# Kernel optimization log

Hardware: AMD Instinct MI355X
Metric: run time of the kernel (lower is better)

## Reference

```python
import jax, jax.numpy as jnp
from jax import lax
import numpy as np

D_MODEL = 256; D_INNER = 512; D_STATE = 16; D_CONV = 4; DT_RANK = 16
B = 2; T = 4096


def _mamba(x, W_in, conv_w, conv_b, W_x, W_dt, b_dt, A_log, D, W_out):
    # Standard mamba_ssm Mamba block (d_state=16, d_conv=4, expand=2).
    b, t, _ = x.shape
    xz = x @ W_in                                   # (B,T,2*d_inner)
    xi, z = jnp.split(xz, 2, axis=-1)
    # causal depthwise conv1d along T
    xc = lax.conv_general_dilated(
        xi.transpose(0, 2, 1), conv_w[:, None, :], (1,),
        [(D_CONV - 1, 0)], dimension_numbers=('NCH', 'OIH', 'NCH'),
        feature_group_count=D_INNER)
    xi = jax.nn.silu(xc.transpose(0, 2, 1) + conv_b)  # (B,T,d_inner)
    xdbl = xi @ W_x                                  # (B,T,dt_rank+2*d_state)
    dt, Bm, Cm = jnp.split(xdbl, [DT_RANK, DT_RANK + D_STATE], axis=-1)
    dt = jax.nn.softplus(dt @ W_dt + b_dt)           # (B,T,d_inner)
    A = -jnp.exp(A_log)                              # (d_inner,d_state)
    dA = jnp.exp(dt[..., None] * A)                  # (B,T,d_inner,d_state)
    dBx = dt[..., None] * Bm[:, :, None, :] * xi[..., None]

    def step(h, ins):
        dA_t, dBx_t, C_t = ins
        h = dA_t * h + dBx_t                         # (B,d_inner,d_state)
        y = jnp.einsum('bdn,bn->bd', h, C_t)
        return h, y

    h0 = jnp.zeros((b, D_INNER, D_STATE), x.dtype)
    _, ys = lax.scan(step, h0,
                     (dA.transpose(1, 0, 2, 3), dBx.transpose(1, 0, 2, 3),
                      Cm.transpose(1, 0, 2)))
    y = ys.transpose(1, 0, 2) + xi * D               # skip connection D*x
    y = y * jax.nn.silu(z)                           # gate
    return y @ W_out                                 # (B,T,d_model)


def _mamba_params(key, prefix):
    ks = jax.random.split(key, 6)
    s = 0.02
    return {
        prefix + "_W_in": jax.random.normal(ks[0], (D_MODEL, 2 * D_INNER)) * s,
        prefix + "_conv_w": jax.random.normal(ks[1], (D_INNER, D_CONV)) * s,
        prefix + "_conv_b": jnp.zeros((D_INNER,), jnp.float32),
        prefix + "_W_x": jax.random.normal(ks[2], (D_INNER, DT_RANK + 2 * D_STATE)) * s,
        prefix + "_W_dt": jax.random.normal(ks[3], (DT_RANK, D_INNER)) * s,
        prefix + "_b_dt": jax.random.normal(ks[4], (D_INNER,)) * s,
        prefix + "_A_log": jnp.log(jnp.tile(jnp.arange(1, D_STATE + 1, dtype=jnp.float32), (D_INNER, 1))),
        prefix + "_D": jnp.ones((D_INNER,), jnp.float32),
        prefix + "_W_out": jax.random.normal(ks[5], (D_INNER, D_MODEL)) * s,
    }


def setup_inputs():
    key = jax.random.key(0)
    kx, kf, kb, km = jax.random.split(key, 4)
    inp = {"x": jax.random.normal(kx, (B, T, D_MODEL), jnp.float32)}
    inp.update(_mamba_params(kf, "fw"))
    inp.update(_mamba_params(kb, "bw"))
    inp["merge_W"] = jax.random.normal(km, (2 * D_MODEL, D_MODEL)) * 0.02
    return inp


def reference(x, fw_W_in, fw_conv_w, fw_conv_b, fw_W_x, fw_W_dt, fw_b_dt, fw_A_log, fw_D, fw_W_out,
              bw_W_in, bw_conv_w, bw_conv_b, bw_W_x, bw_W_dt, bw_b_dt, bw_A_log, bw_D, bw_W_out,
              merge_W):
    out_f = _mamba(x, fw_W_in, fw_conv_w, fw_conv_b, fw_W_x, fw_W_dt, fw_b_dt, fw_A_log, fw_D, fw_W_out)
    out_b = jnp.flip(
        _mamba(jnp.flip(x, 1), bw_W_in, bw_conv_w, bw_conv_b, bw_W_x, bw_W_dt, bw_b_dt, bw_A_log, bw_D, bw_W_out),
        1)
    # dropout is identity in eval mode
    return jnp.concatenate([out_f, out_b], axis=-1) @ merge_W
```

## Files before the change

kernel.cpp:

```cpp
#include <hip/hip_runtime.h>
#include <math.h>

#define T_SEQ 4096
#define ROWS 8192
#define NCHUNK 128
#define CLEN 32

typedef __attribute__((ext_vector_type(4))) float f32x4;
typedef __attribute__((ext_vector_type(2))) float f32x2;
typedef __attribute__((ext_vector_type(8))) short s16x8;

#if __has_builtin(__builtin_elementwise_fma)
#define PKFMA(a, b, c) __builtin_elementwise_fma((a), (b), (c))
#else
#define PKFMA(a, b, c) ((a) * (b) + (c))
#endif

__device__ __forceinline__ float siluf(float x) { return x / (1.f + __expf(-x)); }
__device__ __forceinline__ float softplusf(float x) {
    return fmaxf(x, 0.f) + __logf(1.f + __expf(-fabsf(x)));
}
__device__ __forceinline__ ushort f2b(float f) {
    uint u = __float_as_uint(f);
    u += 0x7fffu + ((u >> 16) & 1u);
    return (ushort)(u >> 16);
}
__device__ __forceinline__ float b2f(ushort h) { return __uint_as_float(((uint)h) << 16); }

__device__ __forceinline__ void gl16(const ushort* g, const char* l)
{
    __builtin_amdgcn_global_load_lds(
        (const __attribute__((address_space(1))) void*)g,
        (__attribute__((address_space(3))) void*)l,
        16, 0, 0);
}

__device__ __forceinline__ void cvt_body(const float* in, ushort* out, int bid, int tid)
{
    int i = bid * 256 + tid;
    const float4* p = reinterpret_cast<const float4*>(in) + (size_t)i * 2;
    float4 a = p[0], b = p[1];
    s16x8 v;
    v[0] = (short)f2b(a.x); v[1] = (short)f2b(a.y); v[2] = (short)f2b(a.z); v[3] = (short)f2b(a.w);
    v[4] = (short)f2b(b.x); v[5] = (short)f2b(b.y); v[6] = (short)f2b(b.z); v[7] = (short)f2b(b.w);
    *reinterpret_cast<s16x8*>(out + (size_t)i * 8) = v;
}

__device__ __forceinline__ void transpose_body(const float* W, ushort* WT,
                                               int Kdim, int Ndim, int bid, int tid)
{
    int idx = bid * 256 + tid;
    int kg8 = Kdim >> 3;
    if (idx >= Ndim * kg8) return;
    int n = idx / kg8, kg = idx - n * kg8;
    s16x8 v;
    #pragma unroll
    for (int i = 0; i < 8; ++i)
        v[i] = (short)f2b(W[(size_t)(kg * 8 + i) * Ndim + n]);
    *reinterpret_cast<s16x8*>(WT + (size_t)n * Kdim + kg * 8) = v;
}

__device__ __forceinline__ void fusew_body(const float* W_out, const float* merge,
                                           ushort* WT, int mrow0, int koff, int bid, int tid)
{
    int idx = bid * 256 + tid;
    int dd = idx >> 8, j = idx & 255;
    float acc = 0.f;
    const float* wr = W_out + dd * 256;
    const float* mc = merge + (size_t)mrow0 * 256 + j;
    #pragma unroll 4
    for (int m = 0; m < 256; ++m)
        acc = fmaf(wr[m], mc[(size_t)m * 256], acc);
    WT[(size_t)j * 1024 + koff + dd] = f2b(acc);
}

__device__ __forceinline__ void wall_body(const float* Wx, const float* Wdt,
                                          ushort* WT, int bid, int tid)
{
    int idx = bid * 256 + tid;
    int n = idx >> 6, kg = idx & 63;
    s16x8 v;
    #pragma unroll
    for (int i = 0; i < 8; ++i) {
        int k = kg * 8 + i;
        float acc = 0.f;
        if (n < 512) {
            #pragma unroll
            for (int j = 0; j < 16; ++j)
                acc = fmaf(Wx[k * 48 + j], Wdt[j * 512 + n], acc);
        } else if (n < 544) {
            acc = Wx[k * 48 + 16 + (n - 512)];
        }
        v[i] = (short)f2b(acc);
    }
    *reinterpret_cast<s16x8*>(WT + (size_t)n * 512 + kg * 8) = v;
}

__global__ __launch_bounds__(256)
void prep_kernel(const float* __restrict__ x,
                 const float* __restrict__ fW_in, const float* __restrict__ bW_in,
                 const float* __restrict__ fW_out, const float* __restrict__ bW_out,
                 const float* __restrict__ merge,
                 const float* __restrict__ fW_x, const float* __restrict__ fW_dt,
                 const float* __restrict__ bW_x, const float* __restrict__ bW_dt,
                 ushort* __restrict__ xbh,
                 ushort* __restrict__ WinT_f, ushort* __restrict__ WinT_b,
                 ushort* __restrict__ WallOut,
                 ushort* __restrict__ Wall_f, ushort* __restrict__ Wall_b)
{
    int bid = blockIdx.x, tid = threadIdx.x;
    if (bid < 1024)        cvt_body(x, xbh, bid, tid);
    else if (bid < 1152)   transpose_body(fW_in, WinT_f, 256, 1024, bid - 1024, tid);
    else if (bid < 1280)   transpose_body(bW_in, WinT_b, 256, 1024, bid - 1152, tid);
    else if (bid < 1792)   fusew_body(fW_out, merge, WallOut, 0, 0, bid - 1280, tid);
    else if (bid < 2304)   fusew_body(bW_out, merge, WallOut, 256, 512, bid - 1792, tid);
    else if (bid < 2464)   wall_body(fW_x, fW_dt, Wall_f, bid - 2304, tid);
    else                   wall_body(bW_x, bW_dt, Wall_b, bid - 2464, tid);
}

template<int BM, int BN, int EPI>
__global__ __launch_bounds__(256)
void mgemm(const ushort* __restrict__ A0, const ushort* __restrict__ A1,
           const ushort* __restrict__ B0, const ushort* __restrict__ B1,
           void* __restrict__ C0, void* __restrict__ C1,
           const float* __restrict__ bias0, const float* __restrict__ bias1,
           float* __restrict__ X0, float* __restrict__ X1,
           int K, int ldc, int flip0, int flip1, int zmode, int nseg)
{
    constexpr int MF = BM / 32, NF = BN / 32;
    constexpr int ASTR = BM / 32, BSTR = BN / 32;
    constexpr int ABYTES = BM * 128;
    __shared__ char lds[BM * 128 + BN * 128];

    const int tid = threadIdx.x;
    const int L = tid & 63, w = tid >> 6;
    const int wm = w >> 1, wn = w & 1;
    const int m0 = blockIdx.y * BM, n0 = blockIdx.x * BN;

    f32x4 acc[MF][NF];
    #pragma unroll
    for (int i = 0; i < MF; ++i)
        #pragma unroll
        for (int j = 0; j < NF; ++j)
            acc[i][j] = (f32x4){0.f, 0.f, 0.f, 0.f};

    const int rsub = L >> 3;
    const int q = (L & 7) ^ rsub;
    const int sb = zmode ? blockIdx.z : 0;
    const int se = zmode ? sb + 1 : nseg;

    for (int s = sb; s < se; ++s) {
        const ushort* Ap = s ? A1 : A0;
        const ushort* Bp = s ? B1 : B0;
        const int flip = s ? flip1 : flip0;

        const ushort* ap[ASTR];
        const ushort* bp[BSTR];
        #pragma unroll
        for (int c = 0; c < ASTR; ++c) {
            int rg = m0 + (w * ASTR + c) * 8 + rsub;
            if (flip) rg ^= (T_SEQ - 1);
            ap[c] = Ap + (size_t)rg * K + q * 8;
        }
        #pragma unroll
        for (int c = 0; c < BSTR; ++c) {
            int ng = n0 + (w * BSTR + c) * 8 + rsub;
            bp[c] = Bp + (size_t)ng * K + q * 8;
        }

        for (int k0 = 0; k0 < K; k0 += 64) {
            #pragma unroll
            for (int c = 0; c < ASTR; ++c) {
                gl16(ap[c], lds + (w * ASTR + c) * 1024);
                ap[c] += 64;
            }
            #pragma unroll
            for (int c = 0; c < BSTR; ++c) {
                gl16(bp[c], lds + ABYTES + (w * BSTR + c) * 1024);
                bp[c] += 64;
            }
            __syncthreads();
            #pragma unroll
            for (int kk = 0; kk < 2; ++kk) {
                const int sw = (((kk * 4 + (L >> 4)) ^ (L & 7)) << 4);
                s16x8 af[MF], bf[NF];
                #pragma unroll
                for (int i = 0; i < MF; ++i) {
                    int R = wm * (BM / 2) + i * 16 + (L & 15);
                    af[i] = *reinterpret_cast<const s16x8*>(lds + R * 128 + sw);
                }
                #pragma unroll
                for (int j = 0; j < NF; ++j) {
                    int R = wn * (BN / 2) + j * 16 + (L & 15);
                    bf[j] = *reinterpret_cast<const s16x8*>(lds + ABYTES + R * 128 + sw);
                }
                #pragma unroll
                for (int i = 0; i < MF; ++i)
                    #pragma unroll
                    for (int j = 0; j < NF; ++j)
                        acc[i][j] = __builtin_amdgcn_mfma_f32_16x16x32_bf16(
                            af[i], bf[j], acc[i][j], 0, 0, 0);
            }
            __syncthreads();
        }
    }

    void* Cv = (zmode && blockIdx.z) ? C1 : C0;
    const float* bias = (zmode && blockIdx.z) ? bias1 : bias0;
    float* Xv = (zmode && blockIdx.z) ? X1 : X0;
    #pragma unroll
    for (int i = 0; i < MF; ++i) {
        #pragma unroll
        for (int j = 0; j < NF; ++j) {
            int r0 = m0 + wm * (BM / 2) + i * 16 + ((L >> 4) << 2);
            int c  = n0 + wn * (BN / 2) + j * 16 + (L & 15);
            if (EPI == 2) {
                if (c < 512) {
                    float bv = bias[c];
                    #pragma unroll
                    for (int r = 0; r < 4; ++r)
                        ((float*)Cv)[(size_t)(r0 + r) * 512 + c] =
                            softplusf(acc[i][j][r] + bv);
                } else if (c < 544) {
                    #pragma unroll
                    for (int r = 0; r < 4; ++r)
                        Xv[(size_t)(r0 + r) * 32 + (c - 512)] = acc[i][j][r];
                }
            } else {
                #pragma unroll
                for (int r = 0; r < 4; ++r) {
                    size_t o = (size_t)(r0 + r) * ldc + c;
                    if (EPI == 1) ((ushort*)Cv)[o] = f2b(acc[i][j][r]);
                    else          ((float*)Cv)[o]  = acc[i][j][r];
                }
            }
        }
    }
}

__global__ __launch_bounds__(256)
void conv_kernel(const ushort* __restrict__ xz_f, const ushort* __restrict__ xz_b,
                 const float* __restrict__ w_f, const float* __restrict__ w_b,
                 const float* __restrict__ bias_f, const float* __restrict__ bias_b,
                 ushort* __restrict__ xi_f, ushort* __restrict__ xi_b)
{
    int g = blockIdx.x * 256 + threadIdx.x;
    int dir = g >> 17;
    int rem = g & 131071;
    int rb = rem >> 7;
    int cg = rem & 127;
    int r0 = rb * 8;
    int d0 = cg * 4;
    int t0 = r0 & (T_SEQ - 1);

    const ushort* xz  = dir ? xz_b : xz_f;
    const float*  w   = dir ? w_b : w_f;
    const float*  bia = dir ? bias_b : bias_f;
    ushort*       xi  = dir ? xi_b : xi_f;

    float wv[4][4], bs[4];
    #pragma unroll
    for (int j = 0; j < 4; ++j) {
        float4 wj = *reinterpret_cast<const float4*>(w + (d0 + j) * 4);
        wv[j][0] = wj.x; wv[j][1] = wj.y; wv[j][2] = wj.z; wv[j][3] = wj.w;
        bs[j] = bia[d0 + j];
    }

    float xv[11][4];
    #pragma unroll
    for (int k = 0; k < 11; ++k) {
        int tt = t0 - 3 + k;
        if (tt >= 0) {
            ushort4 v = *reinterpret_cast<const ushort4*>(
                xz + (size_t)(r0 - 3 + k) * 1024 + d0);
            xv[k][0] = b2f(v.x); xv[k][1] = b2f(v.y);
            xv[k][2] = b2f(v.z); xv[k][3] = b2f(v.w);
        } else {
            xv[k][0] = xv[k][1] = xv[k][2] = xv[k][3] = 0.f;
        }
    }

    #pragma unroll
    for (int t = 0; t < 8; ++t) {
        ushort4 o;
        ushort* op = reinterpret_cast<ushort*>(&o);
        #pragma unroll
        for (int j = 0; j < 4; ++j) {
            float acc = bs[j];
            acc = fmaf(wv[j][0], xv[t + 0][j], acc);
            acc = fmaf(wv[j][1], xv[t + 1][j], acc);
            acc = fmaf(wv[j][2], xv[t + 2][j], acc);
            acc = fmaf(wv[j][3], xv[t + 3][j], acc);
            op[j] = f2b(siluf(acc));
        }
        *reinterpret_cast<ushort4*>(xi + (size_t)(r0 + t) * 512 + d0) = o;
    }
}

__device__ __forceinline__ void scan_head(int bid, int tid,
    int& db, int& b, int& dir, int& chunk, int& d, size_t& row0)
{
    int half = bid & 1;
    int tmp = bid >> 1;
    chunk = tmp & (NCHUNK - 1);
    db = tmp >> 7;
    b = db & 1; dir = db >> 1;
    d = half * 256 + tid;
    row0 = (size_t)b * T_SEQ + (size_t)chunk * CLEN;
}

__device__ __forceinline__ void load_a16(const float* __restrict__ Al, int d,
                                         float* a, bool& fast)
{
    const float4* ap = reinterpret_cast<const float4*>(Al + (size_t)d * 16);
    #pragma unroll
    for (int i = 0; i < 4; ++i) {
        float4 v = ap[i];
        a[4*i+0] = -expf(v.x); a[4*i+1] = -expf(v.y);
        a[4*i+2] = -expf(v.z); a[4*i+3] = -expf(v.w);
    }
    fast = true;
    #pragma unroll
    for (int n = 1; n < 16; ++n)
        fast = fast && (fabsf(a[n] - (float)(n + 1) * a[0]) <= 1e-4f * (float)(n + 1));
}

#define LD16(dst, src_t)                                              \
    {                                                                 \
        const float4* q_ = reinterpret_cast<const float4*>(src_t);    \
        float4 q0 = q_[0], q1 = q_[1], q2 = q_[2], q3 = q_[3];        \
        dst[0]=q0.x; dst[1]=q0.y; dst[2]=q0.z; dst[3]=q0.w;           \
        dst[4]=q1.x; dst[5]=q1.y; dst[6]=q1.z; dst[7]=q1.w;           \
        dst[8]=q2.x; dst[9]=q2.y; dst[10]=q2.z; dst[11]=q2.w;         \
        dst[12]=q3.x; dst[13]=q3.y; dst[14]=q3.z; dst[15]=q3.w;       \
    }

__global__ __launch_bounds__(256)
void scan_pass1(const ushort* __restrict__ xi_f, const ushort* __restrict__ xi_b,
                const float* __restrict__ dt_f, const float* __restrict__ dt_b,
                const float* __restrict__ xd_f, const float* __restrict__ xd_b,
                const float* __restrict__ Al_f, const float* __restrict__ Al_b,
                float* __restrict__ Sdt, float* __restrict__ Hloc)
{
    __shared__ float Bsh[CLEN][16];
    int db, b, dir, chunk, d; size_t row0;
    scan_head(blockIdx.x, threadIdx.x, db, b, dir, chunk, d, row0);

    const ushort* xi = dir ? xi_b : xi_f;
    const float* dt  = dir ? dt_b : dt_f;
    const float* xd  = dir ? xd_b : xd_f;
    const float* Al  = dir ? Al_b : Al_f;

    float a[16]; bool fast;
    load_a16(Al, d, a, fast);

    for (int i = threadIdx.x; i < CLEN * 16; i += 256) {
        int r = i >> 4, n = i & 15;
        Bsh[r][n] = xd[(row0 + r) * 32 + n];
    }
    __syncthreads();

    const ushort* xip = xi + row0 * 512 + d;
    const float*  dtp = dt + row0 * 512 + d;
    float h[16];
    float sumdt = 0.f;

    if (fast) {
        f32x2 h2[8];
        #pragma unroll
        for (int j = 0; j < 8; ++j) h2[j] = (f32x2){0.f, 0.f};
        for (int t = 0; t < CLEN; ++t) {
            float dtv = dtp[(size_t)t * 512];
            float xiv = b2f(xip[(size_t)t * 512]);
            float dbx = dtv * xiv;
            sumdt += dtv;
            float qv = __expf(dtv * a[0]);
            float q2 = qv * qv;
            f32x2 Q2 = (f32x2){q2, q2};
            f32x2 p  = (f32x2){qv, q2};
            f32x2 dbx2 = (f32x2){dbx, dbx};
            const f32x2* bq = reinterpret_cast<const f32x2*>(Bsh[t]);
            #pragma unroll
            for (int j = 0; j < 8; ++j) {
                f32x2 r = bq[j] * dbx2;
                h2[j] = PKFMA(p, h2[j], r);
                if (j < 7) p = p * Q2;
            }
        }
        #pragma unroll
        for (int j = 0; j < 8; ++j) { h[2*j] = h2[j][0]; h[2*j+1] = h2[j][1]; }
    } else {
        #pragma unroll
        for (int n = 0; n < 16; ++n) h[n] = 0.f;
        for (int t = 0; t < CLEN; ++t) {
            float bn[16]; LD16(bn, Bsh[t]);
            float dtv = dtp[(size_t)t * 512];
            float xiv = b2f(xip[(size_t)t * 512]);
            float dbx = dtv * xiv;
            sumdt += dtv;
            #pragma unroll
            for (int n = 0; n < 16; ++n) {
                float dA = __expf(dtv * a[n]);
                h[n] = fmaf(dA, h[n], dbx * bn[n]);
            }
        }
    }

    Sdt[((size_t)db * NCHUNK + chunk) * 512 + d] = sumdt;
    size_t si = ((size_t)((db * NCHUNK + chunk) * 512 + d)) * 16;
    float4* Ho = reinterpret_cast<float4*>(Hloc + si);
    #pragma unroll
    for (int i = 0; i < 4; ++i)
        Ho[i] = make_float4(h[4*i+0], h[4*i+1], h[4*i+2], h[4*i+3]);
}

__global__ __launch_bounds__(256)
void scan_pass2(const float* __restrict__ Sdt, const float* __restrict__ Hloc,
                const float* __restrict__ Al_f, const float* __restrict__ Al_b,
                float* __restrict__ Hin)
{
    int tid = blockIdx.x * 256 + threadIdx.x;
    int db = tid >> 13;
    int dn = tid & 8191;
    int d = dn >> 4;
    const float* Al = (db >> 1) ? Al_b : Al_f;
    float a = -expf(Al[dn]);

    size_t hbase = (size_t)db * NCHUNK * 8192 + dn;
    size_t sbase = (size_t)db * NCHUNK * 512 + d;
    float h = 0.f;
    #pragma unroll 4
    for (int c = 0; c < NCHUNK; ++c) {
        Hin[hbase + (size_t)c * 8192] = h;
        float dA = __expf(a * Sdt[sbase + (size_t)c * 512]);
        h = fmaf(dA, h, Hloc[hbase + (size_t)c * 8192]);
    }
}

__global__ __launch_bounds__(256)
void scan_pass3(const ushort* __restrict__ xi_f, const ushort* __restrict__ xi_b,
                const float* __restrict__ dt_f, const float* __restrict__ dt_b,
                const float* __restrict__ xd_f, const float* __restrict__ xd_b,
                const float* __restrict__ Al_f, const float* __restrict__ Al_b,
                const ushort* __restrict__ xz_f, const ushort* __restrict__ xz_b,
                const float* __restrict__ D_f, const float* __restrict__ D_b,
                const float* __restrict__ Hin,
                ushort* __restrict__ y_all)
{
    __shared__ float Bsh[CLEN][16];
    __shared__ float Csh[CLEN][16];
    int db, b, dir, chunk, d; size_t row0;
    scan_head(blockIdx.x, threadIdx.x, db, b, dir, chunk, d, row0);

    const ushort* xi = dir ? xi_b : xi_f;
    const float* dt  = dir ? dt_b : dt_f;
    const float* xd  = dir ? xd_b : xd_f;
    const float* Al  = dir ? Al_b : Al_f;
    const ushort* xz = dir ? xz_b : xz_f;
    const float* Dv  = dir ? D_b  : D_f;

    float a[16]; bool fast;
    load_a16(Al, d, a, fast);
    float Dd = Dv[d];

    for (int i = threadIdx.x; i < CLEN * 32; i += 256) {
        int r = i >> 5, c = i & 31;
        float v = xd[(row0 + r) * 32 + c];
        if (c < 16) Bsh[r][c] = v; else Csh[r][c - 16] = v;
    }
    __syncthreads();

    const ushort* xip = xi + row0 * 512 + d;
    const float*  dtp = dt + row0 * 512 + d;
    const ushort* zp  = xz + row0 * 1024 + 512 + d;

    ushort* yp;
    long ystep;
    if (dir == 0) {
        yp = y_all + row0 * 1024 + d;
        ystep = 1024;
    } else {
        size_t rowu = (size_t)b * T_SEQ + (T_SEQ - 1) - (size_t)chunk * CLEN;
        yp = y_all + rowu * 1024 + 512 + d;
        ystep = -1024;
    }

    size_t si = ((size_t)((db * NCHUNK + chunk) * 512 + d)) * 16;

    if (fast) {
        f32x2 h2[8];
        {
            const f32x2* hp = reinterpret_cast<const f32x2*>(Hin + si);
            #pragma unroll
            for (int j = 0; j < 8; ++j) h2[j] = hp[j];
        }
        for (int t = 0; t < CLEN; ++t) {
            float dtv = dtp[(size_t)t * 512];
            float xiv = b2f(xip[(size_t)t * 512]);
            float zv  = b2f(zp[(size_t)t * 1024]);
            float dbx = dtv * xiv;
            float qv = __expf(dtv * a[0]);
            float q2 = qv * qv;
            f32x2 Q2 = (f32x2){q2, q2};
            f32x2 p  = (f32x2){qv, q2};
            f32x2 dbx2 = (f32x2){dbx, dbx};
            f32x2 yac = (f32x2){0.f, 0.f};
            const f32x2* bq = reinterpret_cast<const f32x2*>(Bsh[t]);
            const f32x2* cq = reinterpret_cast<const f32x2*>(Csh[t]);
            #pragma unroll
            for (int j = 0; j < 8; ++j) {
                f32x2 r = bq[j] * dbx2;
                h2[j] = PKFMA(p, h2[j], r);
                yac = PKFMA(h2[j], cq[j], yac);
                if (j < 7) p = p * Q2;
            }
            float yacc = yac[0] + yac[1];
            yp[(long)t * ystep] = f2b(fmaf(xiv, Dd, yacc) * siluf(zv));
        }
    } else {
        float h[16];
        {
            const float4* hp = reinterpret_cast<const float4*>(Hin + si);
            #pragma unroll
            for (int i = 0; i < 4; ++i) {
                float4 v = hp[i];
                h[4*i+0] = v.x; h[4*i+1] = v.y; h[4*i+2] = v.z; h[4*i+3] = v.w;
            }
        }
        for (int t = 0; t < CLEN; ++t) {
            float bn[16]; LD16(bn, Bsh[t]);
            float cn[16]; LD16(cn, Csh[t]);
            float dtv = dtp[(size_t)t * 512];
            float xiv = b2f(xip[(size_t)t * 512]);
            float zv  = b2f(zp[(size_t)t * 1024]);
            float dbx = dtv * xiv;
            float yacc = 0.f;
            #pragma unroll
            for (int n = 0; n < 16; ++n) {
                float dA = __expf(dtv * a[n]);
                h[n] = fmaf(dA, h[n], dbx * bn[n]);
                yacc = fmaf(h[n], cn[n], yacc);
            }
            yp[(long)t * ystep] = f2b(fmaf(xiv, Dd, yacc) * siluf(zv));
        }
    }
}

extern "C" void kernel_launch(void* const* d_in, const int* in_sizes, int n_in,
                              void* d_out, int out_size, void* d_ws, size_t ws_size,
                              hipStream_t stream)
{
    const float* x       = (const float*)d_in[0];
    const float* fW_in   = (const float*)d_in[1];
    const float* fconv_w = (const float*)d_in[2];
    const float* fconv_b = (const float*)d_in[3];
    const float* fW_x    = (const float*)d_in[4];
    const float* fW_dt   = (const float*)d_in[5];
    const float* fb_dt   = (const float*)d_in[6];
    const float* fA_log  = (const float*)d_in[7];
    const float* fD      = (const float*)d_in[8];
    const float* fW_out  = (const float*)d_in[9];
    const float* bW_in   = (const float*)d_in[10];
    const float* bconv_w = (const float*)d_in[11];
    const float* bconv_b = (const float*)d_in[12];
    const float* bW_x    = (const float*)d_in[13];
    const float* bW_dt   = (const float*)d_in[14];
    const float* bb_dt   = (const float*)d_in[15];
    const float* bA_log  = (const float*)d_in[16];
    const float* bD      = (const float*)d_in[17];
    const float* bW_out  = (const float*)d_in[18];
    const float* merge   = (const float*)d_in[19];
    float* out = (float*)d_out;

    char* ws = (char*)d_ws;
    ushort* xbh     = (ushort*)ws; ws += (size_t)ROWS * 256 * 2;
    ushort* WinT_f  = (ushort*)ws; ws += (size_t)1024 * 256 * 2;
    ushort* WinT_b  = (ushort*)ws; ws += (size_t)1024 * 256 * 2;
    ushort* WallOut = (ushort*)ws; ws += (size_t)256 * 1024 * 2;
    ushort* Wall_f  = (ushort*)ws; ws += (size_t)640 * 512 * 2;
    ushort* Wall_b  = (ushort*)ws; ws += (size_t)640 * 512 * 2;
    ushort* xz_f    = (ushort*)ws; ws += (size_t)ROWS * 1024 * 2;
    ushort* xz_b    = (ushort*)ws; ws += (size_t)ROWS * 1024 * 2;
    ushort* xi_f    = (ushort*)ws; ws += (size_t)ROWS * 512 * 2;
    ushort* xi_b    = (ushort*)ws; ws += (size_t)ROWS * 512 * 2;
    ushort* y_all   = (ushort*)ws; ws += (size_t)ROWS * 1024 * 2;
    float*  dt_f    = (float*)ws;  ws += (size_t)ROWS * 512 * 4;
    float*  dt_b    = (float*)ws;  ws += (size_t)ROWS * 512 * 4;
    float*  xd_f    = (float*)ws;  ws += (size_t)ROWS * 32 * 4;
    float*  xd_b    = (float*)ws;  ws += (size_t)ROWS * 32 * 4;
    float*  Sdt     = (float*)ws;  ws += (size_t)4 * NCHUNK * 512 * 4;
    float*  Hloc    = (float*)ws;  ws += (size_t)4 * NCHUNK * 8192 * 4;
    float*  Hin     = (float*)ws;  ws += (size_t)4 * NCHUNK * 8192 * 4;

    dim3 blk(256);

    prep_kernel<<<2624, blk, 0, stream>>>(x, fW_in, bW_in, fW_out, bW_out, merge,
                                          fW_x, fW_dt, bW_x, bW_dt,
                                          xbh, WinT_f, WinT_b, WallOut, Wall_f, Wall_b);

    mgemm<64, 128, 1><<<dim3(8, 128, 2), blk, 0, stream>>>(
        xbh, xbh, WinT_f, WinT_b, xz_f, xz_b, nullptr, nullptr, nullptr, nullptr,
        256, 1024, 0, 1, 1, 1);

    conv_kernel<<<1024, blk, 0, stream>>>(xz_f, xz_b, fconv_w, bconv_w,
                                          fconv_b, bconv_b, xi_f, xi_b);

    mgemm<64, 128, 2><<<dim3(5, 128, 2), blk, 0, stream>>>(
        xi_f, xi_b, Wall_f, Wall_b, dt_f, dt_b, fb_dt, bb_dt, xd_f, xd_b,
        512, 512, 0, 0, 1, 1);

    scan_pass1<<<1024, blk, 0, stream>>>(xi_f, xi_b, dt_f, dt_b, xd_f, xd_b,
                                         fA_log, bA_log, Sdt, Hloc);
    scan_pass2<<<128, blk, 0, stream>>>(Sdt, Hloc, fA_log, bA_log, Hin);
    scan_pass3<<<1024, blk, 0, stream>>>(xi_f, xi_b, dt_f, dt_b, xd_f, xd_b,
                                         fA_log, bA_log, xz_f, xz_b, fD, bD,
                                         Hin, y_all);

    mgemm<64, 64, 0><<<dim3(4, 128, 1), blk, 0, stream>>>(
        y_all, nullptr, WallOut, nullptr, out, nullptr, nullptr, nullptr,
        nullptr, nullptr, 1024, 256, 0, 0, 0, 1);
}
```

Before: 176.1 us.

## Store dt in bf16, merge in-proj GEMMs, and swizzle GEMM block order

The dt activation buffer becomes bf16 instead of fp32. The dt_proj GEMM epilogue writes bf16, and both scan passes convert it back to float on load, which halves dt traffic in three kernels. The forward and backward in_proj GEMMs become one N=2048 GEMM over the unflipped input. It relies on WinT_f and WinT_b sitting next to each other in memory, and the backward half is written to time-flipped rows. A linear block-index swizzle in mgemm groups neighbouring tiles differently, likely to improve cache locality across chiplets. The cost is lower dt precision feeding the exponentials in the scan.

```diff
diff --git a/kernel.cpp b/kernel.cpp
--- a/kernel.cpp
+++ b/kernel.cpp
@@ -135,7 +135,17 @@
     const int tid = threadIdx.x;
     const int L = tid & 63, w = tid >> 6;
     const int wm = w >> 1, wn = w & 1;
-    const int m0 = blockIdx.y * BM, n0 = blockIdx.x * BN;
+
+    const int nbx = gridDim.x, nby = gridDim.y;
+    int lin = blockIdx.x + nbx * (blockIdx.y + nby * blockIdx.z);
+    int nwg = nbx * nby * gridDim.z;
+    int swz = (lin & 7) * (nwg >> 3) + (lin >> 3);
+    int bz = swz / (nbx * nby);
+    int r2 = swz - bz * nbx * nby;
+    int by = r2 / nbx;
+    int bx = r2 - by * nbx;
+
+    const int m0 = by * BM, n0 = bx * BN;
 
     f32x4 acc[MF][NF];
     #pragma unroll
@@ -146,7 +156,7 @@
 
     const int rsub = L >> 3;
     const int q = (L & 7) ^ rsub;
-    const int sb = zmode ? blockIdx.z : 0;
+    const int sb = zmode ? bz : 0;
     const int se = zmode ? sb + 1 : nseg;
 
     for (int s = sb; s < se; ++s) {
@@ -205,9 +215,9 @@
         }
     }
 
-    void* Cv = (zmode && blockIdx.z) ? C1 : C0;
-    const float* bias = (zmode && blockIdx.z) ? bias1 : bias0;
-    float* Xv = (zmode && blockIdx.z) ? X1 : X0;
+    void* Cv = (zmode && bz) ? C1 : C0;
+    const float* bias = (zmode && bz) ? bias1 : bias0;
+    float* Xv = (zmode && bz) ? X1 : X0;
     #pragma unroll
     for (int i = 0; i < MF; ++i) {
         #pragma unroll
@@ -219,20 +229,28 @@
                     float bv = bias[c];
                     #pragma unroll
                     for (int r = 0; r < 4; ++r)
-                        ((float*)Cv)[(size_t)(r0 + r) * 512 + c] =
-                            softplusf(acc[i][j][r] + bv);
+                        ((ushort*)Cv)[(size_t)(r0 + r) * 512 + c] =
+                            f2b(softplusf(acc[i][j][r] + bv));
                 } else if (c < 544) {
                     #pragma unroll
                     for (int r = 0; r < 4; ++r)
                         Xv[(size_t)(r0 + r) * 32 + (c - 512)] = acc[i][j][r];
                 }
+            } else if (EPI == 3) {
+                if (c < 1024) {
+                    #pragma unroll
+                    for (int r = 0; r < 4; ++r)
+                        ((ushort*)C0)[(size_t)(r0 + r) * 1024 + c] = f2b(acc[i][j][r]);
+                } else {
+                    #pragma unroll
+                    for (int r = 0; r < 4; ++r)
+                        ((ushort*)C1)[(size_t)((r0 + r) ^ (T_SEQ - 1)) * 1024 + (c - 1024)] =
+                            f2b(acc[i][j][r]);
+                }
             } else {
                 #pragma unroll
-                for (int r = 0; r < 4; ++r) {
-                    size_t o = (size_t)(r0 + r) * ldc + c;
-                    if (EPI == 1) ((ushort*)Cv)[o] = f2b(acc[i][j][r]);
-                    else          ((float*)Cv)[o]  = acc[i][j][r];
-                }
+                for (int r = 0; r < 4; ++r)
+                    ((float*)Cv)[(size_t)(r0 + r) * ldc + c] = acc[i][j][r];
             }
         }
     }
@@ -337,7 +355,7 @@
 
 __global__ __launch_bounds__(256)
 void scan_pass1(const ushort* __restrict__ xi_f, const ushort* __restrict__ xi_b,
-                const float* __restrict__ dt_f, const float* __restrict__ dt_b,
+                const ushort* __restrict__ dt_f, const ushort* __restrict__ dt_b,
                 const float* __restrict__ xd_f, const float* __restrict__ xd_b,
                 const float* __restrict__ Al_f, const float* __restrict__ Al_b,
                 float* __restrict__ Sdt, float* __restrict__ Hloc)
@@ -347,7 +365,7 @@
     scan_head(blockIdx.x, threadIdx.x, db, b, dir, chunk, d, row0);
 
     const ushort* xi = dir ? xi_b : xi_f;
-    const float* dt  = dir ? dt_b : dt_f;
+    const ushort* dt = dir ? dt_b : dt_f;
     const float* xd  = dir ? xd_b : xd_f;
     const float* Al  = dir ? Al_b : Al_f;
 
@@ -361,7 +379,7 @@
     __syncthreads();
 
     const ushort* xip = xi + row0 * 512 + d;
-    const float*  dtp = dt + row0 * 512 + d;
+    const ushort* dtp = dt + row0 * 512 + d;
     float h[16];
     float sumdt = 0.f;
 
@@ -370,7 +388,7 @@
         #pragma unroll
         for (int j = 0; j < 8; ++j) h2[j] = (f32x2){0.f, 0.f};
         for (int t = 0; t < CLEN; ++t) {
-            float dtv = dtp[(size_t)t * 512];
+            float dtv = b2f(dtp[(size_t)t * 512]);
             float xiv = b2f(xip[(size_t)t * 512]);
             float dbx = dtv * xiv;
             sumdt += dtv;
@@ -394,7 +412,7 @@
         for (int n = 0; n < 16; ++n) h[n] = 0.f;
         for (int t = 0; t < CLEN; ++t) {
             float bn[16]; LD16(bn, Bsh[t]);
-            float dtv = dtp[(size_t)t * 512];
+            float dtv = b2f(dtp[(size_t)t * 512]);
             float xiv = b2f(xip[(size_t)t * 512]);
             float dbx = dtv * xiv;
             sumdt += dtv;
@@ -439,7 +457,7 @@
 
 __global__ __launch_bounds__(256)
 void scan_pass3(const ushort* __restrict__ xi_f, const ushort* __restrict__ xi_b,
-                const float* __restrict__ dt_f, const float* __restrict__ dt_b,
+                const ushort* __restrict__ dt_f, const ushort* __restrict__ dt_b,
                 const float* __restrict__ xd_f, const float* __restrict__ xd_b,
                 const float* __restrict__ Al_f, const float* __restrict__ Al_b,
                 const ushort* __restrict__ xz_f, const ushort* __restrict__ xz_b,
@@ -453,7 +471,7 @@
     scan_head(blockIdx.x, threadIdx.x, db, b, dir, chunk, d, row0);
 
     const ushort* xi = dir ? xi_b : xi_f;
-    const float* dt  = dir ? dt_b : dt_f;
+    const ushort* dt = dir ? dt_b : dt_f;
     const float* xd  = dir ? xd_b : xd_f;
     const float* Al  = dir ? Al_b : Al_f;
     const ushort* xz = dir ? xz_b : xz_f;
@@ -471,7 +489,7 @@
     __syncthreads();
 
     const ushort* xip = xi + row0 * 512 + d;
-    const float*  dtp = dt + row0 * 512 + d;
+    const ushort* dtp = dt + row0 * 512 + d;
     const ushort* zp  = xz + row0 * 1024 + 512 + d;
 
     ushort* yp;
@@ -495,7 +513,7 @@
             for (int j = 0; j < 8; ++j) h2[j] = hp[j];
         }
         for (int t = 0; t < CLEN; ++t) {
-            float dtv = dtp[(size_t)t * 512];
+            float dtv = b2f(dtp[(size_t)t * 512]);
             float xiv = b2f(xip[(size_t)t * 512]);
             float zv  = b2f(zp[(size_t)t * 1024]);
             float dbx = dtv * xiv;
@@ -530,7 +548,7 @@
         for (int t = 0; t < CLEN; ++t) {
             float bn[16]; LD16(bn, Bsh[t]);
             float cn[16]; LD16(cn, Csh[t]);
-            float dtv = dtp[(size_t)t * 512];
+            float dtv = b2f(dtp[(size_t)t * 512]);
             float xiv = b2f(xip[(size_t)t * 512]);
             float zv  = b2f(zp[(size_t)t * 1024]);
             float dbx = dtv * xiv;
@@ -584,8 +602,8 @@
     ushort* xi_f    = (ushort*)ws; ws += (size_t)ROWS * 512 * 2;
     ushort* xi_b    = (ushort*)ws; ws += (size_t)ROWS * 512 * 2;
     ushort* y_all   = (ushort*)ws; ws += (size_t)ROWS * 1024 * 2;
-    float*  dt_f    = (float*)ws;  ws += (size_t)ROWS * 512 * 4;
-    float*  dt_b    = (float*)ws;  ws += (size_t)ROWS * 512 * 4;
+    ushort* dt_f    = (ushort*)ws; ws += (size_t)ROWS * 512 * 2;
+    ushort* dt_b    = (ushort*)ws; ws += (size_t)ROWS * 512 * 2;
     float*  xd_f    = (float*)ws;  ws += (size_t)ROWS * 32 * 4;
     float*  xd_b    = (float*)ws;  ws += (size_t)ROWS * 32 * 4;
     float*  Sdt     = (float*)ws;  ws += (size_t)4 * NCHUNK * 512 * 4;
@@ -598,9 +616,9 @@
                                           fW_x, fW_dt, bW_x, bW_dt,
                                           xbh, WinT_f, WinT_b, WallOut, Wall_f, Wall_b);
 
-    mgemm<64, 128, 1><<<dim3(8, 128, 2), blk, 0, stream>>>(
-        xbh, xbh, WinT_f, WinT_b, xz_f, xz_b, nullptr, nullptr, nullptr, nullptr,
-        256, 1024, 0, 1, 1, 1);
+    mgemm<64, 128, 3><<<dim3(16, 128), blk, 0, stream>>>(
+        xbh, nullptr, WinT_f, nullptr, xz_f, xz_b, nullptr, nullptr, nullptr, nullptr,
+        256, 1024, 0, 0, 0, 1);
 
     conv_kernel<<<1024, blk, 0, stream>>>(xz_f, xz_b, fconv_w, bconv_w,
                                           fconv_b, bconv_b, xi_f, xi_b);
@@ -616,7 +634,7 @@
                                          fA_log, bA_log, xz_f, xz_b, fD, bD,
                                          Hin, y_all);
 
-    mgemm<64, 64, 0><<<dim3(4, 128, 1), blk, 0, stream>>>(
+    mgemm<64, 64, 0><<<dim3(4, 128), blk, 0, stream>>>(
         y_all, nullptr, WallOut, nullptr, out, nullptr, nullptr, nullptr,
         nullptr, nullptr, 1024, 256, 0, 0, 0, 1);
 }
```

After: 168.4 us. 1.05x faster.
